# Performance work log

Hardware: AMD Instinct MI355X
Metric: run time of the kernel (lower is better)

Reference implementation:

```python
import jax, jax.numpy as jnp
import numpy as np

# dims (see shape_source)
E, L, PE = 128, 16, 33          # events, latent dim, time-vector dim (1+16+16)
F, W, HOP, C = 256, 512, 256, 257  # gen frames, window, hop, rfft coeffs
H, NL, GP = 512, 4, 128         # hidden, n_layers, generator pos channels
N = F * HOP                     # segment samples = 65536
TOTAL = 1048576                 # model total_samples
F2 = 2 * F                      # scheduling frames over padded (2*N) window


def _time_vec(t):
    # time_vector(): rows = [t, sin(t*f), cos(t*f)] -> (33, n)
    t = t.reshape(1, -1)
    fr = jnp.linspace(1.0, TOTAL / 2, PE // 2)[:, None]
    return jnp.concatenate([t, jnp.sin(t * fr), jnp.cos(t * fr)], axis=0)


def setup_inputs() -> dict:
    key = jax.random.key(0)
    ks = jax.random.split(key, 12)
    std = 0.05
    # learned per-event time vectors (pre-masked to the segment window)
    t_ev = jax.random.uniform(ks[0], (E,), minval=-1.0, maxval=1.0)
    times = _time_vec(t_ev).T  # (E, 33)
    # frame positional encodings over the doubled window [early_frame, end_frame]
    s0 = 0.25
    s1 = s0 + (2 * N) / TOTAL
    tpos = jnp.linspace(s0 * 2 * np.pi, s1 * 2 * np.pi, F2)
    pos_encoding = _time_vec(tpos).T[None]  # (1, F2, 33)
    events = jax.random.uniform(ks[1], (E, L), minval=-1.0, maxval=1.0)
    # EventGenerator's decayed random pos-encoding buffer
    pe = jax.random.uniform(ks[2], (1, F, GP), minval=-1.0, maxval=1.0)
    decay = jnp.linspace(1.0, 0.0, F)
    pwr = jax.random.uniform(ks[3], (GP,), minval=10.0, maxval=100.0)
    gen_pos = pe * decay[None, :, None] ** pwr[None, None, :]  # (1, F, GP)
    # uniform(-1,1) noise used by materialize_phase dithering
    dither_noise = jax.random.uniform(ks[4], (1, F, C), minval=-1.0, maxval=1.0)
    w_ee = jax.random.normal(ks[5], (H, L)) * std
    b_ee = jnp.zeros((H,))
    w_ep = jax.random.normal(ks[6], (H, GP)) * std
    b_ep = jnp.zeros((H,))
    net_w = jax.random.normal(ks[7], (NL, H, H)) * std
    net_b = jnp.zeros((NL, H))
    w_mag = jax.random.normal(ks[8], (C, H)) * std
    b_mag = jnp.zeros((C,))
    w_dith = jax.random.normal(ks[9], (C, H)) * std
    b_dith = jnp.zeros((C,))
    return dict(events=events, times=times, pos_encoding=pos_encoding,
                gen_pos=gen_pos, dither_noise=dither_noise,
                w_ee=w_ee, b_ee=b_ee, w_ep=w_ep, b_ep=b_ep,
                net_w=net_w, net_b=net_b, w_mag=w_mag, b_mag=b_mag,
                w_dith=w_dith, b_dith=b_dith)


def reference(events, times, pos_encoding, gen_pos, dither_noise,
              w_ee, b_ee, w_ep, b_ep, net_w, net_b,
              w_mag, b_mag, w_dith, b_dith):
    # ---- EventGenerator ----
    e = events @ w_ee.T + b_ee                  # (E, H)
    p = gen_pos @ w_ep.T + b_ep                 # (1, F, H)
    x = e[:, None, :] + p[0][None]              # (E, F, H)
    for i in range(net_w.shape[0]):
        x = x + jax.nn.selu(x @ net_w[i].T + net_b[i])
    m = jnp.abs(x @ w_mag.T + b_mag)            # (E, F, C)
    d = x @ w_dith.T + b_dith                   # (E, F, C)
    gd = jnp.linspace(0.0, np.pi, C).astype(x.dtype)[None, None, :]
    phase = jnp.cumsum(gd + d * gd * dither_noise, axis=1)  # accumulate over frames
    spec = m * jnp.exp(1j * phase)
    windowed = jnp.fft.irfft(spec, n=W, axis=-1, norm='ortho')  # (E, F, W)
    # overlap-add with hann window, half-lapped (hop = W//2)
    win = (0.5 - 0.5 * jnp.cos(2 * np.pi * jnp.arange(W) / W)).astype(x.dtype)
    windowed = windowed * win
    even = windowed[:, 0::2].reshape(E, -1)     # occupies [0, N)
    odd = windowed[:, 1::2].reshape(E, -1)      # occupies [HOP, N+HOP)
    buf = jnp.zeros((E, N + HOP), dtype=x.dtype)
    buf = buf.at[:, :N].add(even).at[:, HOP:].add(odd)
    samples = buf[:, :N]                        # (E, N)
    # pad with zeros (Model.forward) -> length 2N
    padded = jnp.concatenate([samples, jnp.zeros_like(samples)], axis=-1)
    # ---- schedule_events ----
    sim = jnp.einsum('ed,fd->ef', times, pos_encoding[0])  # (E, F2)
    # sparse_softmax(normalize=True): one-hot of argmax with value 1
    sched = jax.nn.one_hot(jnp.argmax(sim, axis=-1), F2, dtype=padded.dtype)
    # upsample_with_holes: stride HOP, zeros between frames -> (E, 2N)
    sched_up = jnp.pad(sched[..., None], ((0, 0), (0, 0), (0, HOP - 1))).reshape(E, 2 * N)
    # fft_convolve (circular)
    conv = jnp.fft.irfft(jnp.fft.rfft(padded, axis=-1) * jnp.fft.rfft(sched_up, axis=-1),
                         n=2 * N, axis=-1)      # (E, 2N)
    scheduled = jnp.sum(conv, axis=0)[None, None, :]  # (1, 1, 2N)
    return scheduled[:, :, N:]                  # (1, 1, N)
```

## Files before the change

kernel.cpp:

```cpp
#include <hip/hip_runtime.h>
#include <math.h>

#define E_N   128
#define L_N   16
#define PE_N  33
#define F_N   256
#define W_N   512
#define HOP_N 256
#define C_N   257
#define H_N   512
#define GP_N  128
#define F2_N  512
#define NSAMP (F_N*HOP_N)
#define M_ROWS (E_N*F_N)
#define KLD   544
#define MDLD  544
#define WMD_N 640
#define KC    16

#define BM 128
#define BN 128

typedef float f32x4 __attribute__((ext_vector_type(4)));
typedef short s16x8 __attribute__((ext_vector_type(8)));

__device__ __forceinline__ float selu_f(float x){
    const float alpha = 1.6732632423543772f;
    const float scale = 1.0507009873554805f;
    return scale * (x > 0.f ? x : alpha * expm1f(x));
}
__device__ __forceinline__ unsigned short f2bf(float x){
    unsigned u = __float_as_uint(x);
    return (unsigned short)((u + 0x7fffu + ((u >> 16) & 1u)) >> 16);
}
__device__ __forceinline__ float bf2f(unsigned short h){
    return __uint_as_float((unsigned)h << 16);
}
__device__ __forceinline__ void split2(float x, unsigned short* h, unsigned short* l){
    unsigned short hh = f2bf(x);
    *h = hh;
    *l = f2bf(x - bf2f(hh));
}

__global__ __launch_bounds__(256,2) void k_mfma_gemm(
    const unsigned short* __restrict__ Ah, const unsigned short* __restrict__ Al, int lda,
    const unsigned short* __restrict__ Bh, const unsigned short* __restrict__ Bl, int ldb,
    const float* __restrict__ bias,
    unsigned short* __restrict__ Oh, unsigned short* __restrict__ Ol,
    float* __restrict__ Cf, int ldc,
    int K, int mode, int Ncols)
{
    __shared__ unsigned short sm[2][16384];
    const int tid  = threadIdx.x;
    const int w    = tid >> 6;
    const int lane = tid & 63;

    const int gx = gridDim.x;
    const int nwg = gx * gridDim.y;
    const int h = blockIdx.y * gx + blockIdx.x;
    const int t0 = (h & 7) * (nwg >> 3) + (h >> 3);
    const int row0 = (t0 / gx) * BM;
    const int col0 = (t0 - (t0 / gx) * gx) * BN;

    const int wr = w >> 1, wc = w & 1;

    f32x4 acc[4][4] = {};

    int ci_[8], kg_[8], r_[8];
    #pragma unroll
    for (int i = 0; i < 8; ++i) {
        int ci = i*256 + w*64 + lane;
        int c  = ci & 511;
        ci_[i] = ci; kg_[i] = c >> 7; r_[i] = c & 127;
    }

    auto stage = [&](int buf, int k0) {
        #pragma unroll
        for (int i = 0; i < 8; ++i) {
            const unsigned short* gp;
            if      (i < 2) gp = Ah + (size_t)(row0 + r_[i])*lda + (k0 + kg_[i]*8);
            else if (i < 4) gp = Al + (size_t)(row0 + r_[i])*lda + (k0 + kg_[i]*8);
            else if (i < 6) gp = Bh + (size_t)(col0 + r_[i])*ldb + (k0 + kg_[i]*8);
            else            gp = Bl + (size_t)(col0 + r_[i])*ldb + (k0 + kg_[i]*8);
            __builtin_amdgcn_global_load_lds(
                (const __attribute__((address_space(1))) void*)gp,
                (__attribute__((address_space(3))) void*)(&sm[buf][ci_[i]*8]),
                16, 0, 0);
        }
    };

    stage(0, 0);

    const int nt = K >> 5;
    const int kgl = lane >> 4, lr0 = lane & 15;
    for (int t = 0; t < nt; ++t) {
        const int cur = t & 1;
        if (t + 1 < nt) stage(cur ^ 1, (t + 1) << 5);

        if (t + 1 < nt) asm volatile("s_waitcnt vmcnt(8)" ::: "memory");
        else            asm volatile("s_waitcnt vmcnt(0)" ::: "memory");
        __builtin_amdgcn_sched_barrier(0);
        __builtin_amdgcn_s_barrier();

        s16x8 ah[4], al[4], bh[4], bl[4];
        #pragma unroll
        for (int m = 0; m < 4; ++m) {
            int off = (kgl*128 + wr*64 + m*16 + lr0)*8;
            ah[m] = *(const s16x8*)&sm[cur][off];
            al[m] = *(const s16x8*)&sm[cur][4096 + off];
        }
        #pragma unroll
        for (int n = 0; n < 4; ++n) {
            int off = (kgl*128 + wc*64 + n*16 + lr0)*8;
            bh[n] = *(const s16x8*)&sm[cur][8192 + off];
            bl[n] = *(const s16x8*)&sm[cur][12288 + off];
        }
        #pragma unroll
        for (int m = 0; m < 4; ++m)
            #pragma unroll
            for (int n = 0; n < 4; ++n) {
                acc[m][n] = __builtin_amdgcn_mfma_f32_16x16x32_bf16(ah[m], bh[n], acc[m][n], 0,0,0);
                acc[m][n] = __builtin_amdgcn_mfma_f32_16x16x32_bf16(ah[m], bl[n], acc[m][n], 0,0,0);
                acc[m][n] = __builtin_amdgcn_mfma_f32_16x16x32_bf16(al[m], bh[n], acc[m][n], 0,0,0);
            }
        __builtin_amdgcn_s_barrier();
    }

    const int lr = lane & 15, q = lane >> 4;
    if (mode == 0) {
        #pragma unroll
        for (int n = 0; n < 4; ++n) {
            int col = col0 + wc*64 + n*16 + lr;
            float bv = bias[col];
            #pragma unroll
            for (int m = 0; m < 4; ++m) {
                int rb = row0 + wr*64 + m*16 + q*4;
                #pragma unroll
                for (int g = 0; g < 4; ++g) {
                    size_t idx = (size_t)(rb + g)*lda + col;
                    float resid = bf2f(Ah[idx]) + bf2f(Al[idx]);
                    float o = resid + selu_f(acc[m][n][g] + bv);
                    unsigned short hh = f2bf(o);
                    Oh[idx] = hh;
                    Ol[idx] = f2bf(o - bf2f(hh));
                }
            }
        }
    } else if (mode == 1) {
        #pragma unroll
        for (int n = 0; n < 4; ++n) {
            int col = col0 + wc*64 + n*16 + lr;
            if (col < Ncols) {
                float bv = bias[col];
                bool isev = !(col & 1);
                #pragma unroll
                for (int m = 0; m < 4; ++m) {
                    int rb = row0 + wr*64 + m*16 + q*4;
                    #pragma unroll
                    for (int g = 0; g < 4; ++g) {
                        float v = acc[m][n][g] + bv;
                        if (isev) v = fabsf(v);
                        Cf[(size_t)(rb + g)*ldc + col] = v;
                    }
                }
            }
        }
    } else {
        #pragma unroll
        for (int n = 0; n < 4; ++n) {
            int col = col0 + wc*64 + n*16 + lr;
            #pragma unroll
            for (int m = 0; m < 4; ++m) {
                int rb = row0 + wr*64 + m*16 + q*4;
                #pragma unroll
                for (int g = 0; g < 4; ++g)
                    Cf[(size_t)(rb + g)*ldc + col] = acc[m][n][g];
            }
        }
    }
}


__global__ void k_eproj(const float* __restrict__ ev, const float* __restrict__ w,
                        const float* __restrict__ b, float* __restrict__ e_buf){
    int idx = blockIdx.x*256 + threadIdx.x;
    int ei = idx >> 9, h = idx & 511;
    float acc = b[h];
    #pragma unroll
    for (int l = 0; l < L_N; ++l) acc = fmaf(ev[ei*L_N+l], w[h*L_N+l], acc);
    e_buf[idx] = acc;
}

__global__ void k_pproj(const float* __restrict__ gp, const float* __restrict__ w,
                        const float* __restrict__ b, float* __restrict__ p_buf){
    int idx = blockIdx.x*256 + threadIdx.x;
    int f = idx >> 9, h = idx & 511;
    float acc = b[h];
    #pragma unroll 8
    for (int g = 0; g < GP_N; ++g) acc = fmaf(gp[f*GP_N+g], w[h*GP_N+g], acc);
    p_buf[idx] = acc;
}

__global__ void k_xinit_bf(const float4* __restrict__ e_buf, const float4* __restrict__ p_buf,
                           unsigned short* __restrict__ xh, unsigned short* __restrict__ xl){
    int idx = blockIdx.x*256 + threadIdx.x;
    int h4 = idx & 127;
    int r  = idx >> 7;
    int ei = r >> 8, f = r & 255;
    float4 a = e_buf[ei*128 + h4];
    float4 b = p_buf[f*128 + h4];
    float o[4] = {a.x+b.x, a.y+b.y, a.z+b.z, a.w+b.w};
    unsigned short hh[4], ll[4];
    #pragma unroll
    for (int j = 0; j < 4; ++j) split2(o[j], &hh[j], &ll[j]);
    size_t base = (size_t)r*H_N + h4*4;
    *(ushort4*)&xh[base] = make_ushort4(hh[0], hh[1], hh[2], hh[3]);
    *(ushort4*)&xl[base] = make_ushort4(ll[0], ll[1], ll[2], ll[3]);
}

__global__ void k_split4(const float4* __restrict__ src, unsigned short* __restrict__ oh,
                         unsigned short* __restrict__ ol, int n4){
    int i = blockIdx.x*256 + threadIdx.x;
    if (i >= n4) return;
    float4 v = src[i];
    float o[4] = {v.x, v.y, v.z, v.w};
    unsigned short hh[4], ll[4];
    #pragma unroll
    for (int j = 0; j < 4; ++j) split2(o[j], &hh[j], &ll[j]);
    *(ushort4*)&oh[(size_t)i*4] = make_ushort4(hh[0], hh[1], hh[2], hh[3]);
    *(ushort4*)&ol[(size_t)i*4] = make_ushort4(ll[0], ll[1], ll[2], ll[3]);
}

__global__ void k_wmd(const float* __restrict__ wm, const float* __restrict__ wd,
                      const float* __restrict__ bm, const float* __restrict__ bd,
                      unsigned short* __restrict__ wh, unsigned short* __restrict__ wl,
                      float* __restrict__ bmd){
    int idx = blockIdx.x*256 + threadIdx.x;
    if (idx >= WMD_N*H_N) return;
    int m = idx >> 9, h = idx & 511;
    float v = 0.f;
    if (m < 2*C_N) v = (m & 1) ? wd[(m>>1)*H_N + h] : wm[(m>>1)*H_N + h];
    split2(v, &wh[idx], &wl[idx]);
    if (idx < WMD_N) {
        float b = 0.f;
        if (idx < 2*C_N) b = (idx & 1) ? bd[idx>>1] : bm[idx>>1];
        bmd[idx] = b;
    }
}

__global__ void k_basis_bf(unsigned short* __restrict__ bh, unsigned short* __restrict__ bl){
    int idx = blockIdx.x*256 + threadIdx.x;
    if (idx >= F2_N*KLD) return;
    int n = idx / KLD, kr = idx - n*KLD;
    float val = 0.f;
    if (kr < 2*C_N) {
        int k = kr >> 1;
        float wk = (k==0 || k==C_N-1) ? 1.f : 2.f;
        int j = (k*n) & 511;
        float ang = (float)((double)j * 0.01227184630308513);
        float s, c;
        sincosf(ang, &s, &c);
        float wang = (float)((double)n * 0.01227184630308513);
        float win = 0.5f - 0.5f*cosf(wang);
        const float rs = 0.04419417382415922f;
        val = ((kr & 1) ? -s : c) * wk * win * rs;
    }
    split2(val, &bh[idx], &bl[idx]);
}

__global__ void k_sim(const float* __restrict__ times, const float* __restrict__ pos,
                      int* __restrict__ pidx){
    __shared__ float sv[512];
    __shared__ int   si[512];
    int e = blockIdx.x, f = threadIdx.x;
    float acc = 0.f;
    #pragma unroll
    for (int d = 0; d < PE_N; ++d) acc = fmaf(times[e*PE_N+d], pos[f*PE_N+d], acc);
    sv[f] = acc; si[f] = f;
    __syncthreads();
    for (int off = 256; off > 0; off >>= 1) {
        if (f < off) {
            float v2 = sv[f+off]; int i2 = si[f+off];
            if (v2 > sv[f] || (v2 == sv[f] && i2 < si[f])) { sv[f]=v2; si[f]=i2; }
        }
        __syncthreads();
    }
    if (f == 0) pidx[e] = si[0];
}

__global__ void k_phase(const float* __restrict__ md, const float* __restrict__ noise,
                        unsigned short* __restrict__ ch, unsigned short* __restrict__ cl){
    int k0 = blockIdx.x * KC;
    int e  = blockIdx.y;
    int f  = threadIdx.x;
    size_t row = (size_t)(e*F_N + f);

    float mdv[2*KC];
    const float4* mp = (const float4*)(md + row*MDLD + 2*k0);
    #pragma unroll
    for (int i = 0; i < (2*KC)/4; ++i) *(float4*)&mdv[4*i] = mp[i];

    const int lane = f & 63, wv = f >> 6;
    __shared__ float wsum[KC][4];
    float ph[KC];
    #pragma unroll
    for (int kk = 0; kk < KC; ++kk) {
        int k = k0 + kk;
        float p = 0.f;
        if (k < C_N) {
            float d  = mdv[2*kk+1];
            float nz = noise[(size_t)f*C_N + k];
            float gdk = (float)(3.141592653589793/256.0) * (float)k;
            p = gdk + d*gdk*nz;
        }
        #pragma unroll
        for (int off = 1; off < 64; off <<= 1) {
            float t = __shfl_up(p, off);
            if (lane >= off) p += t;
        }
        if (lane == 63) wsum[kk][wv] = p;
        ph[kk] = p;
    }
    __syncthreads();

    unsigned short oh[2*KC], ol[2*KC];
    #pragma unroll
    for (int kk = 0; kk < KC; ++kk) {
        int k = k0 + kk;
        if (k < C_N) {
            float p = ph[kk];
            #pragma unroll
            for (int i = 0; i < 3; ++i) if (i < wv) p += wsum[kk][i];
            float sv, cv;
            sincosf(p, &sv, &cv);
            float m = mdv[2*kk];
            split2(m*cv, &oh[2*kk],   &ol[2*kk]);
            split2(m*sv, &oh[2*kk+1], &ol[2*kk+1]);
        } else {
            oh[2*kk] = 0; oh[2*kk+1] = 0;
            ol[2*kk] = 0; ol[2*kk+1] = 0;
        }
    }
    size_t o = row*KLD + 2*k0;
    #pragma unroll
    for (int i = 0; i < 4; ++i) {
        ((uint4*)(ch + o))[i] = ((const uint4*)oh)[i];
        ((uint4*)(cl + o))[i] = ((const uint4*)ol)[i];
    }
}

__global__ void k_gather(const float* __restrict__ wnd, const int* __restrict__ pidx,
                         float* __restrict__ out){
    __shared__ int sp[E_N];
    int tid = threadIdx.x;
    if (tid < E_N) sp[tid] = pidx[tid]*HOP_N;
    __syncthreads();
    int t = blockIdx.x*256 + tid;
    float acc = 0.f;
    #pragma unroll 4
    for (int e = 0; e < E_N; ++e) {
        int s = t + NSAMP - sp[e];
        if ((unsigned)s < (unsigned)NSAMP) {
            int f1 = s >> 8, n1 = s & 255;
            const float* base = wnd + ((size_t)(e*F_N + f1) << 9);
            acc += base[n1];
            if (f1 > 0) acc += base[n1 + 256 - 512];
        }
    }
    out[t] = acc;
}

extern "C" void kernel_launch(void* const* d_in, const int* in_sizes, int n_in,
                              void* d_out, int out_size, void* d_ws, size_t ws_size,
                              hipStream_t stream) {
    const float* events  = (const float*)d_in[0];
    const float* times   = (const float*)d_in[1];
    const float* pos     = (const float*)d_in[2];
    const float* gen_pos = (const float*)d_in[3];
    const float* noise   = (const float*)d_in[4];
    const float* w_ee    = (const float*)d_in[5];
    const float* b_ee    = (const float*)d_in[6];
    const float* w_ep    = (const float*)d_in[7];
    const float* b_ep    = (const float*)d_in[8];
    const float* net_w   = (const float*)d_in[9];
    const float* net_b   = (const float*)d_in[10];
    const float* w_mag   = (const float*)d_in[11];
    const float* b_mag   = (const float*)d_in[12];
    const float* w_dith  = (const float*)d_in[13];
    const float* b_dith  = (const float*)d_in[14];
    float* out = (float*)d_out;

    char* ws8 = (char*)d_ws;
    unsigned short* xAh = (unsigned short*)(ws8);
    unsigned short* xAl = (unsigned short*)(ws8 + 33554432ull);
    unsigned short* xBh = (unsigned short*)(ws8 + 67108864ull);
    unsigned short* xBl = (unsigned short*)(ws8 + 100663296ull);
    float*          cs32= (float*)(ws8 + 67108864ull);
    unsigned short* csh = (unsigned short*)(ws8);
    unsigned short* csl = (unsigned short*)(ws8 + 138412032ull);
    float*          bufB= (float*)(ws8 + 67108864ull);
    char* sp = ws8 + 174063616ull;
    unsigned short* bash = (unsigned short*)sp;  sp += 557056;
    unsigned short* basl = (unsigned short*)sp;  sp += 557056;
    unsigned short* nwh  = (unsigned short*)sp;  sp += 2097152;
    unsigned short* nwl  = (unsigned short*)sp;  sp += 2097152;
    unsigned short* wmdh = (unsigned short*)sp;  sp += 655360;
    unsigned short* wmdl = (unsigned short*)sp;  sp += 655360;
    float* bmd   = (float*)sp;                   sp += 4096;
    float* e_buf = (float*)sp;                   sp += 262144;
    float* p_buf = (float*)sp;                   sp += 524288;
    int*   pidx  = (int*)sp;

    k_basis_bf<<<(F2_N*KLD + 255)/256, 256, 0, stream>>>(bash, basl);
    k_sim<<<E_N, 512, 0, stream>>>(times, pos, pidx);
    k_split4<<<1024, 256, 0, stream>>>((const float4*)net_w, nwh, nwl, 4*H_N*H_N/4);
    k_wmd<<<(WMD_N*H_N + 255)/256, 256, 0, stream>>>(w_mag, w_dith, b_mag, b_dith, wmdh, wmdl, bmd);
    k_eproj<<<(E_N*H_N)/256, 256, 0, stream>>>(events, w_ee, b_ee, e_buf);
    k_pproj<<<(F_N*H_N)/256, 256, 0, stream>>>(gen_pos, w_ep, b_ep, p_buf);
    k_xinit_bf<<<(M_ROWS*(H_N/4))/256, 256, 0, stream>>>(
        (const float4*)e_buf, (const float4*)p_buf, xAh, xAl);

    unsigned short *ih = xAh, *il = xAl, *oh = xBh, *ol = xBl;
    for (int i = 0; i < 4; ++i) {
        k_mfma_gemm<<<dim3(H_N/BN, M_ROWS/BM), 256, 0, stream>>>(
            ih, il, H_N, nwh + (size_t)i*H_N*H_N, nwl + (size_t)i*H_N*H_N, H_N,
            net_b + (size_t)i*H_N, oh, ol, nullptr, 0, H_N, 0, H_N);
        unsigned short* t;
        t = ih; ih = oh; oh = t;
        t = il; il = ol; ol = t;
    }
    k_mfma_gemm<<<dim3(WMD_N/BN, M_ROWS/BM), 256, 0, stream>>>(
        ih, il, H_N, wmdh, wmdl, H_N, bmd, nullptr, nullptr, cs32, MDLD, H_N, 1, 2*C_N);

    k_phase<<<dim3(17, E_N), 256, 0, stream>>>(cs32, noise, csh, csl);

    k_mfma_gemm<<<dim3(F2_N/BN, M_ROWS/BM), 256, 0, stream>>>(
        csh, csl, KLD, bash, basl, KLD, nullptr, nullptr, nullptr, bufB, W_N, KLD, 3, F2_N);

    k_gather<<<NSAMP/256, 256, 0, stream>>>(bufB, pidx, out);
}
```

Measured before the change: 752.2 us.

## Give each wave a private LDS region in the GEMM to drop block barriers

The MFMA GEMM no longer shares double-buffered A/B tiles across the workgroup. Each wave now stages its own 64-row A and B slices into a private 16 KB LDS region, so both s_barriers per K step go away. Loads for the next step are issued after the current fragments have been read into registers, giving register-level double buffering. The cost is duplicated global traffic: the two waves in a row or column each load the same A or B rows, doubling global/LDS fill per block. There is also less overlap, because each step waits on vmcnt(0).

```diff
diff --git a/kernel.cpp b/kernel.cpp
--- a/kernel.cpp
+++ b/kernel.cpp
@@ -50,7 +50,7 @@
     float* __restrict__ Cf, int ldc,
     int K, int mode, int Ncols)
 {
-    __shared__ unsigned short sm[2][16384];
+    __shared__ unsigned short sm[32768];
     const int tid  = threadIdx.x;
     const int w    = tid >> 6;
     const int lane = tid & 63;
@@ -63,67 +63,61 @@
     const int col0 = (t0 - (t0 / gx) * gx) * BN;
 
     const int wr = w >> 1, wc = w & 1;
+    unsigned short* smw = &sm[w * 8192];
+
+    const int arow = row0 + wr*64 + lane;
+    const int brow = col0 + wc*64 + lane;
 
     f32x4 acc[4][4] = {};
 
-    int ci_[8], kg_[8], r_[8];
-    #pragma unroll
-    for (int i = 0; i < 8; ++i) {
-        int ci = i*256 + w*64 + lane;
-        int c  = ci & 511;
-        ci_[i] = ci; kg_[i] = c >> 7; r_[i] = c & 127;
-    }
-
-    auto stage = [&](int buf, int k0) {
-        #pragma unroll
-        for (int i = 0; i < 8; ++i) {
-            const unsigned short* gp;
-            if      (i < 2) gp = Ah + (size_t)(row0 + r_[i])*lda + (k0 + kg_[i]*8);
-            else if (i < 4) gp = Al + (size_t)(row0 + r_[i])*lda + (k0 + kg_[i]*8);
-            else if (i < 6) gp = Bh + (size_t)(col0 + r_[i])*ldb + (k0 + kg_[i]*8);
-            else            gp = Bl + (size_t)(col0 + r_[i])*ldb + (k0 + kg_[i]*8);
+    auto stage = [&](int k0) {
+        #pragma unroll
+        for (int i = 0; i < 4; ++i) {
             __builtin_amdgcn_global_load_lds(
-                (const __attribute__((address_space(1))) void*)gp,
-                (__attribute__((address_space(3))) void*)(&sm[buf][ci_[i]*8]),
-                16, 0, 0);
+                (const __attribute__((address_space(1))) void*)(Ah + (size_t)arow*lda + k0 + i*8),
+                (__attribute__((address_space(3))) void*)(&smw[(i*64 + lane)*8]), 16, 0, 0);
+            __builtin_amdgcn_global_load_lds(
+                (const __attribute__((address_space(1))) void*)(Al + (size_t)arow*lda + k0 + i*8),
+                (__attribute__((address_space(3))) void*)(&smw[2048 + (i*64 + lane)*8]), 16, 0, 0);
+            __builtin_amdgcn_global_load_lds(
+                (const __attribute__((address_space(1))) void*)(Bh + (size_t)brow*ldb + k0 + i*8),
+                (__attribute__((address_space(3))) void*)(&smw[4096 + (i*64 + lane)*8]), 16, 0, 0);
+            __builtin_amdgcn_global_load_lds(
+                (const __attribute__((address_space(1))) void*)(Bl + (size_t)brow*ldb + k0 + i*8),
+                (__attribute__((address_space(3))) void*)(&smw[6144 + (i*64 + lane)*8]), 16, 0, 0);
         }
     };
 
-    stage(0, 0);
+    stage(0);
 
     const int nt = K >> 5;
     const int kgl = lane >> 4, lr0 = lane & 15;
     for (int t = 0; t < nt; ++t) {
-        const int cur = t & 1;
-        if (t + 1 < nt) stage(cur ^ 1, (t + 1) << 5);
-
-        if (t + 1 < nt) asm volatile("s_waitcnt vmcnt(8)" ::: "memory");
-        else            asm volatile("s_waitcnt vmcnt(0)" ::: "memory");
+        asm volatile("s_waitcnt vmcnt(0)" ::: "memory");
         __builtin_amdgcn_sched_barrier(0);
-        __builtin_amdgcn_s_barrier();
-
-        s16x8 ah[4], al[4], bh[4], bl[4];
+
+        s16x8 ahf[4], alf[4], bhf[4], blf[4];
         #pragma unroll
         for (int m = 0; m < 4; ++m) {
-            int off = (kgl*128 + wr*64 + m*16 + lr0)*8;
-            ah[m] = *(const s16x8*)&sm[cur][off];
-            al[m] = *(const s16x8*)&sm[cur][4096 + off];
-        }
-        #pragma unroll
-        for (int n = 0; n < 4; ++n) {
-            int off = (kgl*128 + wc*64 + n*16 + lr0)*8;
-            bh[n] = *(const s16x8*)&sm[cur][8192 + off];
-            bl[n] = *(const s16x8*)&sm[cur][12288 + off];
-        }
+            int off = (kgl*64 + m*16 + lr0)*8;
+            ahf[m] = *(const s16x8*)&smw[off];
+            alf[m] = *(const s16x8*)&smw[2048 + off];
+            bhf[m] = *(const s16x8*)&smw[4096 + off];
+            blf[m] = *(const s16x8*)&smw[6144 + off];
+        }
+        asm volatile("s_waitcnt lgkmcnt(0)" ::: "memory");
+        __builtin_amdgcn_sched_barrier(0);
+        if (t + 1 < nt) stage((t + 1) << 5);
+        __builtin_amdgcn_sched_barrier(0);
+
         #pragma unroll
         for (int m = 0; m < 4; ++m)
             #pragma unroll
             for (int n = 0; n < 4; ++n) {
-                acc[m][n] = __builtin_amdgcn_mfma_f32_16x16x32_bf16(ah[m], bh[n], acc[m][n], 0,0,0);
-                acc[m][n] = __builtin_amdgcn_mfma_f32_16x16x32_bf16(ah[m], bl[n], acc[m][n], 0,0,0);
-                acc[m][n] = __builtin_amdgcn_mfma_f32_16x16x32_bf16(al[m], bh[n], acc[m][n], 0,0,0);
+                acc[m][n] = __builtin_amdgcn_mfma_f32_16x16x32_bf16(ahf[m], bhf[n], acc[m][n], 0,0,0);
+                acc[m][n] = __builtin_amdgcn_mfma_f32_16x16x32_bf16(ahf[m], blf[n], acc[m][n], 0,0,0);
+                acc[m][n] = __builtin_amdgcn_mfma_f32_16x16x32_bf16(alf[m], bhf[n], acc[m][n], 0,0,0);
             }
-        __builtin_amdgcn_s_barrier();
     }
 
     const int lr = lane & 15, q = lane >> 4;
```

Measured after the change: 1.659 ms. +120.5%, slower.
